# Optimization experiments

Measured on AMD Instinct MI355X. Metric: run time of the kernel, lower is better.

The kernel has to match this reference:

```python
import jax, jax.numpy as jnp
import numpy as np

B, S, D, H = 4, 2048, 1024, 16
DK = D // H


def setup_inputs() -> dict:
    key = jax.random.key(0)
    ks = jax.random.split(key, 12)
    std = 1.0 / np.sqrt(D)
    inp = {
        "q": jax.random.normal(ks[0], (B, S, D), jnp.float32),
        "k": jax.random.normal(ks[1], (B, S, D), jnp.float32),
        "v": jax.random.normal(ks[2], (B, S, D), jnp.float32),
        "mask": jnp.tril(jnp.ones((S, S), jnp.int32))[None, None],  # [1,1,S,S] causal
        "Wq": jax.random.normal(ks[3], (D, D), jnp.float32) * std,
        "bq": jax.random.normal(ks[4], (D,), jnp.float32) * std,
        "Wk": jax.random.normal(ks[5], (D, D), jnp.float32) * std,
        "bk": jax.random.normal(ks[6], (D,), jnp.float32) * std,
        "Wv": jax.random.normal(ks[7], (D, D), jnp.float32) * std,
        "bv": jax.random.normal(ks[8], (D,), jnp.float32) * std,
        "Wo": jax.random.normal(ks[9], (D, D), jnp.float32) * std,
        "bo": jax.random.normal(ks[10], (D,), jnp.float32) * std,
    }
    return inp


def reference(q, k, v, mask, Wq, bq, Wk, bk, Wv, bv, Wo, bo):
    scale = DK ** -0.5
    # linear projections (torch Linear: x @ W.T + b), split into heads -> [B,H,S,DK]
    qh = (q @ Wq.T + bq).reshape(B, S, H, DK).transpose(0, 2, 1, 3)
    kh = (k @ Wk.T + bk).reshape(B, S, H, DK).transpose(0, 2, 1, 3)
    vh = (v @ Wv.T + bv).reshape(B, S, H, DK).transpose(0, 2, 1, 3)
    scores = jnp.einsum("bhqd,bhkd->bhqk", qh, kh) * scale  # [B,H,S,S]
    scores = jnp.where(mask == 0, -1e9, scores)
    attn = jax.nn.softmax(scores, axis=-1)
    ctx = jnp.einsum("bhqk,bhkd->bhqd", attn, vh)
    ctx = ctx.transpose(0, 2, 1, 3).reshape(B, S, D)
    return ctx @ Wo.T + bo
```

## Files before the change

### kernel.cpp

```cpp
#include <hip/hip_runtime.h>
#include <cstdint>

#define DEVI __device__ __forceinline__

typedef short  bfx8 __attribute__((ext_vector_type(8)));
typedef float  fx4  __attribute__((ext_vector_type(4)));
typedef unsigned short u16;
typedef unsigned short usx4 __attribute__((ext_vector_type(4)));
typedef unsigned short usx8 __attribute__((ext_vector_type(8)));

constexpr int Bb = 4, Ss = 2048, Dd = 1024, Hh = 16, DKk = 64;
constexpr int Mtok = Bb * Ss;
constexpr int Kdim = 1024, Ndim = 1024;

DEVI u16 f2b(float f) {
  unsigned u = __builtin_bit_cast(unsigned, f);
  unsigned r = u + 0x7fffu + ((u >> 16) & 1u);
  return (u16)(r >> 16);
}

DEVI void lds16(const void* gptr, void* lptr) {
  __builtin_amdgcn_global_load_lds(
      reinterpret_cast<const __attribute__((address_space(1))) unsigned int*>(
          reinterpret_cast<uintptr_t>(gptr)),
      reinterpret_cast<__attribute__((address_space(3))) unsigned int*>(
          reinterpret_cast<uintptr_t>(lptr)),
      16, 0, 0);
}

DEVI fx4 mfma16(bfx8 a, bfx8 b, fx4 c) {
  return __builtin_amdgcn_mfma_f32_16x16x32_bf16(a, b, c, 0, 0, 0);
}

__global__ __launch_bounds__(256) void f2bf_kernel(const float* __restrict__ in,
                                                   u16* __restrict__ out, int n8) {
  int i = blockIdx.x * blockDim.x + threadIdx.x;
  if (i < n8) {
    const fx4* p = reinterpret_cast<const fx4*>(in + (size_t)i * 8);
    fx4 a = p[0], b = p[1];
    usx8 o;
#pragma unroll
    for (int j = 0; j < 4; ++j) { o[j] = f2b(a[j]); o[4 + j] = f2b(b[j]); }
    *reinterpret_cast<usx8*>(out + (size_t)i * 8) = o;
  }
}

__global__ __launch_bounds__(256) void f2bf4_kernel(const float* __restrict__ i0,
                                                    const float* __restrict__ i1,
                                                    const float* __restrict__ i2,
                                                    const float* __restrict__ i3,
                                                    u16* __restrict__ o0,
                                                    u16* __restrict__ o1,
                                                    u16* __restrict__ o2,
                                                    u16* __restrict__ o3, int n8) {
  const float* in = blockIdx.y == 0 ? i0 : blockIdx.y == 1 ? i1 : blockIdx.y == 2 ? i2 : i3;
  u16* out = blockIdx.y == 0 ? o0 : blockIdx.y == 1 ? o1 : blockIdx.y == 2 ? o2 : o3;
  int i = blockIdx.x * blockDim.x + threadIdx.x;
  if (i < n8) {
    const fx4* p = reinterpret_cast<const fx4*>(in + (size_t)i * 8);
    fx4 a = p[0], b = p[1];
    usx8 o;
#pragma unroll
    for (int j = 0; j < 4; ++j) { o[j] = f2b(a[j]); o[4 + j] = f2b(b[j]); }
    *reinterpret_cast<usx8*>(out + (size_t)i * 8) = o;
  }
}

template <int MODE>
__global__ __launch_bounds__(256) void gemm_bt(const u16* __restrict__ A,
                                               const u16* __restrict__ Bw,
                                               const float* __restrict__ bias,
                                               void* __restrict__ outp, float scale) {
  __shared__ u16 As[128 * 32];
  __shared__ u16 Bs[128 * 32];
  __shared__ u16 Ct[MODE == 1 ? 128 * 132 : 1];

  const int tid = threadIdx.x, w = tid >> 6, l = tid & 63;
  const int g = l >> 4, ln = l & 15;
  const int wr = w >> 1, wc = w & 1;
  const int row0 = blockIdx.y * 128, col0 = blockIdx.x * 128;

  fx4 acc[4][4];
#pragma unroll
  for (int i = 0; i < 4; ++i)
#pragma unroll
    for (int j = 0; j < 4; ++j) acc[i][j] = 0.0f;

  const int srow = w * 32 + (l >> 2);
  const int scol = (l & 3) * 8;

  for (int kt = 0; kt < Kdim; kt += 32) {
#pragma unroll
    for (int i = 0; i < 2; ++i) {
      int r = srow + i * 16;
      lds16(A + (size_t)(row0 + r) * Kdim + kt + scol, As + w * 1024 + i * 512);
      lds16(Bw + (size_t)(col0 + r) * Kdim + kt + scol, Bs + w * 1024 + i * 512);
    }
    __syncthreads();
    bfx8 af[4], bf[4];
#pragma unroll
    for (int mf = 0; mf < 4; ++mf)
      af[mf] = *reinterpret_cast<const bfx8*>(As + (wr * 64 + mf * 16 + ln) * 32 + g * 8);
#pragma unroll
    for (int nf = 0; nf < 4; ++nf)
      bf[nf] = *reinterpret_cast<const bfx8*>(Bs + (wc * 64 + nf * 16 + ln) * 32 + g * 8);
#pragma unroll
    for (int mf = 0; mf < 4; ++mf)
#pragma unroll
      for (int nf = 0; nf < 4; ++nf) acc[mf][nf] = mfma16(af[mf], bf[nf], acc[mf][nf]);
    __syncthreads();
  }

  float bcol[4];
#pragma unroll
  for (int nf = 0; nf < 4; ++nf) bcol[nf] = bias[col0 + wc * 64 + nf * 16 + ln];

  if constexpr (MODE == 0) {
    u16* out = (u16*)outp;
#pragma unroll
    for (int mf = 0; mf < 4; ++mf)
#pragma unroll
      for (int i = 0; i < 4; ++i) {
        int r = row0 + wr * 64 + mf * 16 + g * 4 + i;
        int b = r >> 11, s = r & 2047;
#pragma unroll
        for (int nf = 0; nf < 4; ++nf) {
          int c = col0 + wc * 64 + nf * 16 + ln;
          float v = (acc[mf][nf][i] + bcol[nf]) * scale;
          out[(size_t)(b * Hh + (c >> 6)) * Ss * DKk + (size_t)s * DKk + (c & 63)] = f2b(v);
        }
      }
  } else if constexpr (MODE == 2) {
    float* out = (float*)outp;
#pragma unroll
    for (int mf = 0; mf < 4; ++mf)
#pragma unroll
      for (int i = 0; i < 4; ++i) {
        int r = row0 + wr * 64 + mf * 16 + g * 4 + i;
#pragma unroll
        for (int nf = 0; nf < 4; ++nf) {
          int c = col0 + wc * 64 + nf * 16 + ln;
          out[(size_t)r * Ndim + c] = acc[mf][nf][i] + bcol[nf];
        }
      }
  } else {
#pragma unroll
    for (int mf = 0; mf < 4; ++mf)
#pragma unroll
      for (int i = 0; i < 4; ++i) {
        int rl = wr * 64 + mf * 16 + g * 4 + i;
#pragma unroll
        for (int nf = 0; nf < 4; ++nf)
          Ct[rl * 132 + wc * 64 + nf * 16 + ln] = f2b(acc[mf][nf][i] + bcol[nf]);
      }
    __syncthreads();
    u16* out = (u16*)outp;
    int nloc = tid >> 1;
#pragma unroll
    for (int jj = 0; jj < 8; ++jj) {
      int rl = (tid & 1) * 64 + jj * 8;
      usx8 vv;
#pragma unroll
      for (int e = 0; e < 8; ++e) vv[e] = Ct[(rl + e) * 132 + nloc];
      *reinterpret_cast<usx8*>(out + (size_t)(col0 + nloc) * Mtok + row0 + rl) = vv;
    }
  }
}

__global__ __launch_bounds__(256) void attn_fwd(const u16* __restrict__ qh,
                                                const u16* __restrict__ kh,
                                                const u16* __restrict__ vt,
                                                u16* __restrict__ ctx) {
  __shared__ u16 Ks[64 * 64];
  __shared__ u16 Vts[64 * 64];
  __shared__ u16 Pl[4][32 * 72];

  const int tid = threadIdx.x, w = tid >> 6, l = tid & 63;
  const int g = l >> 4, ln = l & 15;
  const int qt = blockIdx.x, bh = blockIdx.y;
  const int q0 = qt * 128, qw0 = q0 + w * 32;
  const int b = bh >> 4, h = bh & 15;

  const u16* qhead = qh + (size_t)bh * Ss * DKk;
  const u16* khead = kh + (size_t)bh * Ss * DKk;
  const u16* vhead = vt + (size_t)(h * 64) * Mtok + (size_t)b * Ss;

  bfx8 qf_[2][2];
#pragma unroll
  for (int qf = 0; qf < 2; ++qf)
#pragma unroll
    for (int ks = 0; ks < 2; ++ks)
      qf_[qf][ks] = *reinterpret_cast<const bfx8*>(
          qhead + (size_t)(qw0 + qf * 16 + ln) * 64 + ks * 32 + g * 8);

  float m_run[2] = {-1e30f, -1e30f}, l_run[2] = {0.f, 0.f};
  fx4 cacc[2][4];
#pragma unroll
  for (int qf = 0; qf < 2; ++qf)
#pragma unroll
    for (int df = 0; df < 4; ++df) cacc[qf][df] = 0.0f;

  const int ntiles = qt * 2 + 2;
  for (int t = 0; t < ntiles; ++t) {
    const int kt0 = t * 64;
#pragma unroll
    for (int i = 0; i < 2; ++i) {
      int c = i * 256 + tid;
      int kv = c >> 3, dkb = 8 * ((c & 7) ^ (kv & 7));
      lds16(khead + (size_t)(kt0 + kv) * 64 + dkb, Ks + i * 2048 + w * 512);
      int dk = c >> 3, kvb = 8 * ((c & 7) ^ (dk & 7));
      lds16(vhead + (size_t)dk * Mtok + kt0 + kvb, Vts + i * 2048 + w * 512);
    }
    __syncthreads();

    if (kt0 <= qw0 + 31) {
      fx4 sacc[4][2];
#pragma unroll
      for (int kf = 0; kf < 4; ++kf)
#pragma unroll
        for (int qf = 0; qf < 2; ++qf) sacc[kf][qf] = 0.0f;

#pragma unroll
      for (int ks = 0; ks < 2; ++ks) {
        bfx8 kf_[4];
#pragma unroll
        for (int kf = 0; kf < 4; ++kf)
          kf_[kf] = *reinterpret_cast<const bfx8*>(
              Ks + (kf * 16 + ln) * 64 + ((g * 8 + ks * 32) ^ (8 * (ln & 7))));
#pragma unroll
        for (int kf = 0; kf < 4; ++kf)
#pragma unroll
          for (int qf = 0; qf < 2; ++qf)
            sacc[kf][qf] = mfma16(kf_[kf], qf_[qf][ks], sacc[kf][qf]);
      }

      if (kt0 + 63 > qw0) {
#pragma unroll
        for (int kf = 0; kf < 4; ++kf)
#pragma unroll
          for (int qf = 0; qf < 2; ++qf)
#pragma unroll
            for (int i = 0; i < 4; ++i) {
              int kvg = kt0 + kf * 16 + g * 4 + i;
              int qg = qw0 + qf * 16 + ln;
              if (kvg > qg) sacc[kf][qf][i] = -1e30f;
            }
      }

      float rfac[2];
#pragma unroll
      for (int qf = 0; qf < 2; ++qf) {
        float pm = -1e30f;
#pragma unroll
        for (int kf = 0; kf < 4; ++kf)
#pragma unroll
          for (int i = 0; i < 4; ++i) pm = fmaxf(pm, sacc[kf][qf][i]);
        pm = fmaxf(pm, __shfl_xor(pm, 16));
        pm = fmaxf(pm, __shfl_xor(pm, 32));
        float mnew = fmaxf(m_run[qf], pm);
        float r = __builtin_amdgcn_exp2f(m_run[qf] - mnew);
        float ps = 0.f;
#pragma unroll
        for (int kf = 0; kf < 4; ++kf)
#pragma unroll
          for (int i = 0; i < 4; ++i) {
            float p = __builtin_amdgcn_exp2f(sacc[kf][qf][i] - mnew);
            sacc[kf][qf][i] = p;
            ps += p;
          }
        l_run[qf] = l_run[qf] * r + ps;
        m_run[qf] = mnew;
        rfac[qf] = r;
      }

#pragma unroll
      for (int kf = 0; kf < 4; ++kf)
#pragma unroll
        for (int qf = 0; qf < 2; ++qf) {
          usx4 pw;
#pragma unroll
          for (int i = 0; i < 4; ++i) pw[i] = f2b(sacc[kf][qf][i]);
          *reinterpret_cast<usx4*>(&Pl[w][(qf * 16 + ln) * 72 + kf * 16 + g * 4]) = pw;
        }

      float rb[2][4];
#pragma unroll
      for (int qf = 0; qf < 2; ++qf)
#pragma unroll
        for (int i = 0; i < 4; ++i) rb[qf][i] = __shfl(rfac[qf], g * 4 + i);
#pragma unroll
      for (int qf = 0; qf < 2; ++qf)
#pragma unroll
        for (int df = 0; df < 4; ++df)
#pragma unroll
          for (int i = 0; i < 4; ++i) cacc[qf][df][i] *= rb[qf][i];

#pragma unroll
      for (int ks = 0; ks < 2; ++ks) {
        bfx8 pa[2], vb[4];
#pragma unroll
        for (int qf = 0; qf < 2; ++qf)
          pa[qf] = *reinterpret_cast<const bfx8*>(
              &Pl[w][(qf * 16 + ln) * 72 + ks * 32 + g * 8]);
#pragma unroll
        for (int df = 0; df < 4; ++df)
          vb[df] = *reinterpret_cast<const bfx8*>(
              Vts + (df * 16 + ln) * 64 + ((g * 8 + ks * 32) ^ (8 * (ln & 7))));
#pragma unroll
        for (int qf = 0; qf < 2; ++qf)
#pragma unroll
          for (int df = 0; df < 4; ++df)
            cacc[qf][df] = mfma16(pa[qf], vb[df], cacc[qf][df]);
      }
    }
    __syncthreads();
  }

#pragma unroll
  for (int qf = 0; qf < 2; ++qf) {
    float ls = l_run[qf];
    ls += __shfl_xor(ls, 16);
    ls += __shfl_xor(ls, 32);
    l_run[qf] = ls;
  }
  float linv[2][4];
#pragma unroll
  for (int qf = 0; qf < 2; ++qf)
#pragma unroll
    for (int i = 0; i < 4; ++i) linv[qf][i] = 1.0f / __shfl(l_run[qf], g * 4 + i);

#pragma unroll
  for (int qf = 0; qf < 2; ++qf)
#pragma unroll
    for (int df = 0; df < 4; ++df)
#pragma unroll
      for (int i = 0; i < 4; ++i) {
        int qg = q0 + w * 32 + qf * 16 + g * 4 + i;
        int n = h * 64 + df * 16 + ln;
        ctx[(size_t)(b * Ss + qg) * Dd + n] = f2b(cacc[qf][df][i] * linv[qf][i]);
      }
}

extern "C" void kernel_launch(void* const* d_in, const int* in_sizes, int n_in,
                              void* d_out, int out_size, void* d_ws, size_t ws_size,
                              hipStream_t stream) {
  if (ws_size < (size_t)(72u << 20)) return;

  const float* q  = (const float*)d_in[0];
  const float* k  = (const float*)d_in[1];
  const float* v  = (const float*)d_in[2];
  const float* Wq = (const float*)d_in[4];
  const float* bq = (const float*)d_in[5];
  const float* Wk = (const float*)d_in[6];
  const float* bk = (const float*)d_in[7];
  const float* Wv = (const float*)d_in[8];
  const float* bv = (const float*)d_in[9];
  const float* Wo = (const float*)d_in[10];
  const float* bo = (const float*)d_in[11];

  char* ws = (char*)d_ws;
  u16* xb  = (u16*)(ws);
  u16* ctw = (u16*)(ws);
  u16* wbq = (u16*)(ws + (16u << 20));
  u16* wbk = (u16*)(ws + (18u << 20));
  u16* wbv = (u16*)(ws + (20u << 20));
  u16* wbo = (u16*)(ws + (22u << 20));
  u16* qhw = (u16*)(ws + (24u << 20));
  u16* khw = (u16*)(ws + (40u << 20));
  u16* vtw = (u16*)(ws + (56u << 20));

  const int nX8 = Mtok * Dd / 8;
  const int nW8 = Dd * Dd / 8;
  dim3 blk(256);
  dim3 gx((nX8 + 255) / 256);
  dim3 gw4((nW8 + 255) / 256, 4);
  dim3 gemmgrid(Ndim / 128, Mtok / 128);

  f2bf4_kernel<<<gw4, blk, 0, stream>>>(Wq, Wk, Wv, Wo, wbq, wbk, wbv, wbo, nW8);

  const float qscale = 0.125f * 1.44269504088896340736f;

  f2bf_kernel<<<gx, blk, 0, stream>>>(q, xb, nX8);
  gemm_bt<0><<<gemmgrid, blk, 0, stream>>>(xb, wbq, bq, qhw, qscale);
  f2bf_kernel<<<gx, blk, 0, stream>>>(k, xb, nX8);
  gemm_bt<0><<<gemmgrid, blk, 0, stream>>>(xb, wbk, bk, khw, 1.0f);
  f2bf_kernel<<<gx, blk, 0, stream>>>(v, xb, nX8);
  gemm_bt<1><<<gemmgrid, blk, 0, stream>>>(xb, wbv, bv, vtw, 1.0f);

  attn_fwd<<<dim3(Ss / 128, Bb * Hh), blk, 0, stream>>>(qhw, khw, vtw, ctw);

  gemm_bt<2><<<gemmgrid, blk, 0, stream>>>(ctw, wbo, bo, d_out, 1.0f);
}
```

Before: 436.6 us.

## Batch QKV projections, drop LDS staging in attention, remap blocks per XCD

```diff
diff --git a/kernel.cpp b/kernel.cpp
--- a/kernel.cpp
+++ b/kernel.cpp
@@ -66,6 +66,25 @@
   }
 }
 
+__global__ __launch_bounds__(256) void f2bf3_kernel(const float* __restrict__ i0,
+                                                    const float* __restrict__ i1,
+                                                    const float* __restrict__ i2,
+                                                    u16* __restrict__ o0,
+                                                    u16* __restrict__ o1,
+                                                    u16* __restrict__ o2, int n8) {
+  const float* in = blockIdx.y == 0 ? i0 : blockIdx.y == 1 ? i1 : i2;
+  u16* out = blockIdx.y == 0 ? o0 : blockIdx.y == 1 ? o1 : o2;
+  int i = blockIdx.x * blockDim.x + threadIdx.x;
+  if (i < n8) {
+    const fx4* p = reinterpret_cast<const fx4*>(in + (size_t)i * 8);
+    fx4 a = p[0], b = p[1];
+    usx8 o;
+#pragma unroll
+    for (int j = 0; j < 4; ++j) { o[j] = f2b(a[j]); o[4 + j] = f2b(b[j]); }
+    *reinterpret_cast<usx8*>(out + (size_t)i * 8) = o;
+  }
+}
+
 template <int MODE>
 __global__ __launch_bounds__(256) void gemm_bt(const u16* __restrict__ A,
                                                const u16* __restrict__ Bw,
@@ -167,17 +186,122 @@
   }
 }
 
+__global__ __launch_bounds__(256) void gemm_qkv(
+    const u16* __restrict__ xq, const u16* __restrict__ xk, const u16* __restrict__ xv,
+    const u16* __restrict__ wq, const u16* __restrict__ wk, const u16* __restrict__ wv,
+    const float* __restrict__ bq, const float* __restrict__ bk, const float* __restrict__ bv,
+    u16* __restrict__ outq, u16* __restrict__ outk, u16* __restrict__ outv, float qscale) {
+  __shared__ u16 As[128 * 32];
+  __shared__ u16 Bs[128 * 32];
+  __shared__ u16 Ct[32 * 132];
+
+  const int z = blockIdx.z;
+  const u16* A  = z == 0 ? xq : z == 1 ? xk : xv;
+  const u16* Bw = z == 0 ? wq : z == 1 ? wk : wv;
+  const float* bias = z == 0 ? bq : z == 1 ? bk : bv;
+  const float scale = z == 0 ? qscale : 1.0f;
+
+  const int tid = threadIdx.x, w = tid >> 6, l = tid & 63;
+  const int g = l >> 4, ln = l & 15;
+  const int wr = w >> 1, wc = w & 1;
+  const int row0 = blockIdx.y * 128, col0 = blockIdx.x * 128;
+
+  fx4 acc[4][4];
+#pragma unroll
+  for (int i = 0; i < 4; ++i)
+#pragma unroll
+    for (int j = 0; j < 4; ++j) acc[i][j] = 0.0f;
+
+  const int srow = w * 32 + (l >> 2);
+  const int scol = (l & 3) * 8;
+
+  for (int kt = 0; kt < Kdim; kt += 32) {
+#pragma unroll
+    for (int i = 0; i < 2; ++i) {
+      int r = srow + i * 16;
+      lds16(A + (size_t)(row0 + r) * Kdim + kt + scol, As + w * 1024 + i * 512);
+      lds16(Bw + (size_t)(col0 + r) * Kdim + kt + scol, Bs + w * 1024 + i * 512);
+    }
+    __syncthreads();
+    bfx8 af[4], bf[4];
+#pragma unroll
+    for (int mf = 0; mf < 4; ++mf)
+      af[mf] = *reinterpret_cast<const bfx8*>(As + (wr * 64 + mf * 16 + ln) * 32 + g * 8);
+#pragma unroll
+    for (int nf = 0; nf < 4; ++nf)
+      bf[nf] = *reinterpret_cast<const bfx8*>(Bs + (wc * 64 + nf * 16 + ln) * 32 + g * 8);
+#pragma unroll
+    for (int mf = 0; mf < 4; ++mf)
+#pragma unroll
+      for (int nf = 0; nf < 4; ++nf) acc[mf][nf] = mfma16(af[mf], bf[nf], acc[mf][nf]);
+    __syncthreads();
+  }
+
+  float bcol[4];
+#pragma unroll
+  for (int nf = 0; nf < 4; ++nf) bcol[nf] = bias[col0 + wc * 64 + nf * 16 + ln];
+
+  if (z < 2) {
+    u16* out = z == 0 ? outq : outk;
+#pragma unroll
+    for (int mf = 0; mf < 4; ++mf)
+#pragma unroll
+      for (int i = 0; i < 4; ++i) {
+        int r = row0 + wr * 64 + mf * 16 + g * 4 + i;
+        int b = r >> 11, s = r & 2047;
+#pragma unroll
+        for (int nf = 0; nf < 4; ++nf) {
+          int c = col0 + wc * 64 + nf * 16 + ln;
+          float v = (acc[mf][nf][i] + bcol[nf]) * scale;
+          out[(size_t)(b * Hh + (c >> 6)) * Ss * DKk + (size_t)s * DKk + (c & 63)] = f2b(v);
+        }
+      }
+  } else {
+    u16* out = outv;
+    const int nloc = tid >> 1, hh = tid & 1;
+#pragma unroll
+    for (int cc = 0; cc < 4; ++cc) {
+      __syncthreads();
+      if (wr == (cc >> 1)) {
+#pragma unroll
+        for (int mm = 0; mm < 2; ++mm) {
+          int mf = (cc & 1) * 2 + mm;
+#pragma unroll
+          for (int i = 0; i < 4; ++i) {
+            int lrow = mm * 16 + g * 4 + i;
+#pragma unroll
+            for (int nf = 0; nf < 4; ++nf)
+              Ct[lrow * 132 + wc * 64 + nf * 16 + ln] = f2b(acc[mf][nf][i] + bcol[nf]);
+          }
+        }
+      }
+      __syncthreads();
+#pragma unroll
+      for (int jj = 0; jj < 2; ++jj) {
+        int rbase = hh * 16 + jj * 8;
+        usx8 vv;
+#pragma unroll
+        for (int e = 0; e < 8; ++e) vv[e] = Ct[(rbase + e) * 132 + nloc];
+        *reinterpret_cast<usx8*>(out + (size_t)(col0 + nloc) * Mtok + row0 + cc * 32 + rbase) = vv;
+      }
+    }
+  }
+}
+
 __global__ __launch_bounds__(256) void attn_fwd(const u16* __restrict__ qh,
                                                 const u16* __restrict__ kh,
                                                 const u16* __restrict__ vt,
                                                 u16* __restrict__ ctx) {
-  __shared__ u16 Ks[64 * 64];
-  __shared__ u16 Vts[64 * 64];
   __shared__ u16 Pl[4][32 * 72];
 
   const int tid = threadIdx.x, w = tid >> 6, l = tid & 63;
   const int g = l >> 4, ln = l & 15;
-  const int qt = blockIdx.x, bh = blockIdx.y;
+
+  const int id = blockIdx.x + (blockIdx.y << 4);
+  const int xcd = id & 7, j = id >> 3;
+  const int bh = xcd * 8 + (j >> 4);
+  const int qt = 15 - (j & 15);
+
   const int q0 = qt * 128, qw0 = q0 + w * 32;
   const int b = bh >> 4, h = bh & 15;
 
@@ -200,120 +324,108 @@
 #pragma unroll
     for (int df = 0; df < 4; ++df) cacc[qf][df] = 0.0f;
 
-  const int ntiles = qt * 2 + 2;
-  for (int t = 0; t < ntiles; ++t) {
+  const int ntw = ((qw0 + 31) >> 6) + 1;
+  for (int t = 0; t < ntw; ++t) {
     const int kt0 = t * 64;
-#pragma unroll
-    for (int i = 0; i < 2; ++i) {
-      int c = i * 256 + tid;
-      int kv = c >> 3, dkb = 8 * ((c & 7) ^ (kv & 7));
-      lds16(khead + (size_t)(kt0 + kv) * 64 + dkb, Ks + i * 2048 + w * 512);
-      int dk = c >> 3, kvb = 8 * ((c & 7) ^ (dk & 7));
-      lds16(vhead + (size_t)dk * Mtok + kt0 + kvb, Vts + i * 2048 + w * 512);
-    }
-    __syncthreads();
-
-    if (kt0 <= qw0 + 31) {
-      fx4 sacc[4][2];
+
+    fx4 sacc[4][2];
+#pragma unroll
+    for (int kf = 0; kf < 4; ++kf)
+#pragma unroll
+      for (int qf = 0; qf < 2; ++qf) sacc[kf][qf] = 0.0f;
+
+#pragma unroll
+    for (int ks = 0; ks < 2; ++ks) {
+      bfx8 kf_[4];
 #pragma unroll
       for (int kf = 0; kf < 4; ++kf)
-#pragma unroll
-        for (int qf = 0; qf < 2; ++qf) sacc[kf][qf] = 0.0f;
-
-#pragma unroll
-      for (int ks = 0; ks < 2; ++ks) {
-        bfx8 kf_[4];
-#pragma unroll
-        for (int kf = 0; kf < 4; ++kf)
-          kf_[kf] = *reinterpret_cast<const bfx8*>(
-              Ks + (kf * 16 + ln) * 64 + ((g * 8 + ks * 32) ^ (8 * (ln & 7))));
-#pragma unroll
-        for (int kf = 0; kf < 4; ++kf)
-#pragma unroll
-          for (int qf = 0; qf < 2; ++qf)
-            sacc[kf][qf] = mfma16(kf_[kf], qf_[qf][ks], sacc[kf][qf]);
-      }
-
-      if (kt0 + 63 > qw0) {
-#pragma unroll
-        for (int kf = 0; kf < 4; ++kf)
-#pragma unroll
-          for (int qf = 0; qf < 2; ++qf)
-#pragma unroll
-            for (int i = 0; i < 4; ++i) {
-              int kvg = kt0 + kf * 16 + g * 4 + i;
-              int qg = qw0 + qf * 16 + ln;
-              if (kvg > qg) sacc[kf][qf][i] = -1e30f;
-            }
-      }
-
-      float rfac[2];
+        kf_[kf] = *reinterpret_cast<const bfx8*>(
+            khead + (size_t)(kt0 + kf * 16 + ln) * 64 + ks * 32 + g * 8);
+#pragma unroll
+      for (int kf = 0; kf < 4; ++kf)
+#pragma unroll
+        for (int qf = 0; qf < 2; ++qf)
+          sacc[kf][qf] = mfma16(kf_[kf], qf_[qf][ks], sacc[kf][qf]);
+    }
+
+    if (kt0 + 63 > qw0) {
+#pragma unroll
+      for (int kf = 0; kf < 4; ++kf)
+#pragma unroll
+        for (int qf = 0; qf < 2; ++qf)
+#pragma unroll
+          for (int i = 0; i < 4; ++i) {
+            int kvg = kt0 + kf * 16 + g * 4 + i;
+            int qg = qw0 + qf * 16 + ln;
+            if (kvg > qg) sacc[kf][qf][i] = -1e30f;
+          }
+    }
+
+    float rfac[2];
+#pragma unroll
+    for (int qf = 0; qf < 2; ++qf) {
+      float pm = -1e30f;
+#pragma unroll
+      for (int kf = 0; kf < 4; ++kf)
+#pragma unroll
+        for (int i = 0; i < 4; ++i) pm = fmaxf(pm, sacc[kf][qf][i]);
+      pm = fmaxf(pm, __shfl_xor(pm, 16));
+      pm = fmaxf(pm, __shfl_xor(pm, 32));
+      float mnew = fmaxf(m_run[qf], pm);
+      float r = __builtin_amdgcn_exp2f(m_run[qf] - mnew);
+      float ps = 0.f;
+#pragma unroll
+      for (int kf = 0; kf < 4; ++kf)
+#pragma unroll
+        for (int i = 0; i < 4; ++i) {
+          float p = __builtin_amdgcn_exp2f(sacc[kf][qf][i] - mnew);
+          sacc[kf][qf][i] = p;
+          ps += p;
+        }
+      l_run[qf] = l_run[qf] * r + ps;
+      m_run[qf] = mnew;
+      rfac[qf] = r;
+    }
+
+#pragma unroll
+    for (int kf = 0; kf < 4; ++kf)
 #pragma unroll
       for (int qf = 0; qf < 2; ++qf) {
-        float pm = -1e30f;
-#pragma unroll
-        for (int kf = 0; kf < 4; ++kf)
-#pragma unroll
-          for (int i = 0; i < 4; ++i) pm = fmaxf(pm, sacc[kf][qf][i]);
-        pm = fmaxf(pm, __shfl_xor(pm, 16));
-        pm = fmaxf(pm, __shfl_xor(pm, 32));
-        float mnew = fmaxf(m_run[qf], pm);
-        float r = __builtin_amdgcn_exp2f(m_run[qf] - mnew);
-        float ps = 0.f;
-#pragma unroll
-        for (int kf = 0; kf < 4; ++kf)
-#pragma unroll
-          for (int i = 0; i < 4; ++i) {
-            float p = __builtin_amdgcn_exp2f(sacc[kf][qf][i] - mnew);
-            sacc[kf][qf][i] = p;
-            ps += p;
-          }
-        l_run[qf] = l_run[qf] * r + ps;
-        m_run[qf] = mnew;
-        rfac[qf] = r;
-      }
-
-#pragma unroll
-      for (int kf = 0; kf < 4; ++kf)
-#pragma unroll
-        for (int qf = 0; qf < 2; ++qf) {
-          usx4 pw;
-#pragma unroll
-          for (int i = 0; i < 4; ++i) pw[i] = f2b(sacc[kf][qf][i]);
-          *reinterpret_cast<usx4*>(&Pl[w][(qf * 16 + ln) * 72 + kf * 16 + g * 4]) = pw;
-        }
-
-      float rb[2][4];
+        usx4 pw;
+#pragma unroll
+        for (int i = 0; i < 4; ++i) pw[i] = f2b(sacc[kf][qf][i]);
+        *reinterpret_cast<usx4*>(&Pl[w][(qf * 16 + ln) * 72 + kf * 16 + g * 4]) = pw;
+      }
+
+    float rb[2][4];
+#pragma unroll
+    for (int qf = 0; qf < 2; ++qf)
+#pragma unroll
+      for (int i = 0; i < 4; ++i) rb[qf][i] = __shfl(rfac[qf], g * 4 + i);
+#pragma unroll
+    for (int qf = 0; qf < 2; ++qf)
+#pragma unroll
+      for (int df = 0; df < 4; ++df)
+#pragma unroll
+        for (int i = 0; i < 4; ++i) cacc[qf][df][i] *= rb[qf][i];
+
+#pragma unroll
+    for (int ks = 0; ks < 2; ++ks) {
+      bfx8 pa[2], vb[4];
 #pragma unroll
       for (int qf = 0; qf < 2; ++qf)
-#pragma unroll
-        for (int i = 0; i < 4; ++i) rb[qf][i] = __shfl(rfac[qf], g * 4 + i);
+        pa[qf] = *reinterpret_cast<const bfx8*>(
+            &Pl[w][(qf * 16 + ln) * 72 + ks * 32 + g * 8]);
+#pragma unroll
+      for (int df = 0; df < 4; ++df)
+        vb[df] = *reinterpret_cast<const bfx8*>(
+            vhead + (size_t)(df * 16 + ln) * Mtok + kt0 + ks * 32 + g * 8);
 #pragma unroll
       for (int qf = 0; qf < 2; ++qf)
 #pragma unroll
         for (int df = 0; df < 4; ++df)
-#pragma unroll
-          for (int i = 0; i < 4; ++i) cacc[qf][df][i] *= rb[qf][i];
-
-#pragma unroll
-      for (int ks = 0; ks < 2; ++ks) {
-        bfx8 pa[2], vb[4];
-#pragma unroll
-        for (int qf = 0; qf < 2; ++qf)
-          pa[qf] = *reinterpret_cast<const bfx8*>(
-              &Pl[w][(qf * 16 + ln) * 72 + ks * 32 + g * 8]);
-#pragma unroll
-        for (int df = 0; df < 4; ++df)
-          vb[df] = *reinterpret_cast<const bfx8*>(
-              Vts + (df * 16 + ln) * 64 + ((g * 8 + ks * 32) ^ (8 * (ln & 7))));
-#pragma unroll
-        for (int qf = 0; qf < 2; ++qf)
-#pragma unroll
-          for (int df = 0; df < 4; ++df)
-            cacc[qf][df] = mfma16(pa[qf], vb[df], cacc[qf][df]);
-      }
-    }
-    __syncthreads();
+          cacc[qf][df] = mfma16(pa[qf], vb[df], cacc[qf][df]);
+    }
   }
 
 #pragma unroll
@@ -359,35 +471,58 @@
   const float* bo = (const float*)d_in[11];
 
   char* ws = (char*)d_ws;
-  u16* xb  = (u16*)(ws);
-  u16* ctw = (u16*)(ws);
-  u16* wbq = (u16*)(ws + (16u << 20));
-  u16* wbk = (u16*)(ws + (18u << 20));
-  u16* wbv = (u16*)(ws + (20u << 20));
-  u16* wbo = (u16*)(ws + (22u << 20));
-  u16* qhw = (u16*)(ws + (24u << 20));
-  u16* khw = (u16*)(ws + (40u << 20));
-  u16* vtw = (u16*)(ws + (56u << 20));
-
   const int nX8 = Mtok * Dd / 8;
   const int nW8 = Dd * Dd / 8;
   dim3 blk(256);
   dim3 gx((nX8 + 255) / 256);
   dim3 gw4((nW8 + 255) / 256, 4);
   dim3 gemmgrid(Ndim / 128, Mtok / 128);
-
-  f2bf4_kernel<<<gw4, blk, 0, stream>>>(Wq, Wk, Wv, Wo, wbq, wbk, wbv, wbo, nW8);
-
   const float qscale = 0.125f * 1.44269504088896340736f;
 
-  f2bf_kernel<<<gx, blk, 0, stream>>>(q, xb, nX8);
-  gemm_bt<0><<<gemmgrid, blk, 0, stream>>>(xb, wbq, bq, qhw, qscale);
-  f2bf_kernel<<<gx, blk, 0, stream>>>(k, xb, nX8);
-  gemm_bt<0><<<gemmgrid, blk, 0, stream>>>(xb, wbk, bk, khw, 1.0f);
-  f2bf_kernel<<<gx, blk, 0, stream>>>(v, xb, nX8);
-  gemm_bt<1><<<gemmgrid, blk, 0, stream>>>(xb, wbv, bv, vtw, 1.0f);
-
-  attn_fwd<<<dim3(Ss / 128, Bb * Hh), blk, 0, stream>>>(qhw, khw, vtw, ctw);
-
-  gemm_bt<2><<<gemmgrid, blk, 0, stream>>>(ctw, wbo, bo, d_out, 1.0f);
-}
+  if (ws_size >= (size_t)(104u << 20)) {
+    u16* xq  = (u16*)(ws);
+    u16* xk  = (u16*)(ws + (16u << 20));
+    u16* xv  = (u16*)(ws + (32u << 20));
+    u16* wbq = (u16*)(ws + (48u << 20));
+    u16* wbk = (u16*)(ws + (50u << 20));
+    u16* wbv = (u16*)(ws + (52u << 20));
+    u16* wbo = (u16*)(ws + (54u << 20));
+    u16* qhw = (u16*)(ws + (56u << 20));
+    u16* khw = (u16*)(ws + (72u << 20));
+    u16* vtw = (u16*)(ws + (88u << 20));
+    u16* ctw = (u16*)(ws);
+
+    f2bf4_kernel<<<gw4, blk, 0, stream>>>(Wq, Wk, Wv, Wo, wbq, wbk, wbv, wbo, nW8);
+    f2bf3_kernel<<<dim3((nX8 + 255) / 256, 3), blk, 0, stream>>>(q, k, v, xq, xk, xv, nX8);
+
+    gemm_qkv<<<dim3(Ndim / 128, Mtok / 128, 3), blk, 0, stream>>>(
+        xq, xk, xv, wbq, wbk, wbv, bq, bk, bv, qhw, khw, vtw, qscale);
+
+    attn_fwd<<<dim3(Ss / 128, Bb * Hh), blk, 0, stream>>>(qhw, khw, vtw, ctw);
+
+    gemm_bt<2><<<gemmgrid, blk, 0, stream>>>(ctw, wbo, bo, d_out, 1.0f);
+  } else {
+    u16* xb  = (u16*)(ws);
+    u16* ctw = (u16*)(ws);
+    u16* wbq = (u16*)(ws + (16u << 20));
+    u16* wbk = (u16*)(ws + (18u << 20));
+    u16* wbv = (u16*)(ws + (20u << 20));
+    u16* wbo = (u16*)(ws + (22u << 20));
+    u16* qhw = (u16*)(ws + (24u << 20));
+    u16* khw = (u16*)(ws + (40u << 20));
+    u16* vtw = (u16*)(ws + (56u << 20));
+
+    f2bf4_kernel<<<gw4, blk, 0, stream>>>(Wq, Wk, Wv, Wo, wbq, wbk, wbv, wbo, nW8);
+
+    f2bf_kernel<<<gx, blk, 0, stream>>>(q, xb, nX8);
+    gemm_bt<0><<<gemmgrid, blk, 0, stream>>>(xb, wbq, bq, qhw, qscale);
+    f2bf_kernel<<<gx, blk, 0, stream>>>(k, xb, nX8);
+    gemm_bt<0><<<gemmgrid, blk, 0, stream>>>(xb, wbk, bk, khw, 1.0f);
+    f2bf_kernel<<<gx, blk, 0, stream>>>(v, xb, nX8);
+    gemm_bt<1><<<gemmgrid, blk, 0, stream>>>(xb, wbv, bv, vtw, 1.0f);
+
+    attn_fwd<<<dim3(Ss / 128, Bb * Hh), blk, 0, stream>>>(qhw, khw, vtw, ctw);
+
+    gemm_bt<2><<<gemmgrid, blk, 0, stream>>>(ctw, wbo, bo, d_out, 1.0f);
+  }
+}
```

New measurement: 460.0 us. 1.05x slower.
